# Performance work log

Measured on AMD Instinct MI355X. Metric: run time of the kernel, lower is better.

The kernel has to match this reference:

```python
import jax, jax.numpy as jnp
import numpy as np

B, S, H, D, DM = 2, 512, 8, 32, 256  # batch, seq_len, n_head, d_k, d_model


def setup_inputs() -> dict:
    key = jax.random.key(0)
    ks = jax.random.split(key, 8)
    scale = 0.02
    return {
        "hidden_states": jax.random.normal(ks[0], (B, S, DM), dtype=jnp.float32),
        "rpe": jax.random.normal(ks[1], (B, S, S, D), dtype=jnp.float32),
        "w_q": jax.random.normal(ks[2], (DM, H * D), dtype=jnp.float32) * scale,
        "w_k": jax.random.normal(ks[3], (DM, H * D), dtype=jnp.float32) * scale,
        "w_v": jax.random.normal(ks[4], (DM, H * D), dtype=jnp.float32) * scale,
        "fc_w": jax.random.normal(ks[5], (H * D, DM), dtype=jnp.float32) * scale,
        "fc_b": jnp.zeros((DM,), dtype=jnp.float32),
        "ln_w": jnp.ones((DM,), dtype=jnp.float32),
        "ln_b": jnp.zeros((DM,), dtype=jnp.float32),
        "station_num": 256,
    }


def reference(hidden_states, rpe, w_q, w_k, w_v, fc_w, fc_b, ln_w, ln_b, station_num):
    b, s, dm = hidden_states.shape
    d = rpe.shape[-1]
    h = w_q.shape[1] // d

    def heads(x, w):
        # (b, s, dm) @ (dm, h*d) -> (b, h, s, d)
        return (x @ w).reshape(b, s, h, d).transpose(0, 2, 1, 3)

    q = heads(hidden_states, w_q)
    k = heads(hidden_states, w_k)
    v = heads(hidden_states, w_v)

    # torch: (q.unsqueeze(2) * k.unsqueeze(3) * rpe.unsqueeze(1)).sum(-1)
    # scores[b,h,i,j] = sum_d q[b,h,j,d] * k[b,h,i,d] * rpe[b,i,j,d]
    scores = jnp.einsum('bhjd,bhid,bijd->bhij', q, k, rpe) / jnp.sqrt(jnp.float32(d))

    # shielded mask: column j visible if j < station_num, plus the diagonal
    col = jnp.arange(s) < station_num                  # (s,)
    mask = col[None, :] | jnp.eye(s, dtype=bool)        # (s, s)
    scores = jnp.where(mask[None, None], scores, jnp.float32(-1e10))

    attn = jax.nn.softmax(scores, axis=-1)              # (b, h, s, s)
    out = jnp.einsum('bhij,bhjd->bhid', attn, v)        # (b, h, s, d)
    out = out.transpose(0, 2, 1, 3).reshape(b, s, h * d)

    ctx = out @ fc_w + fc_b + hidden_states             # residual
    mu = jnp.mean(ctx, axis=-1, keepdims=True)
    var = jnp.mean(jnp.square(ctx - mu), axis=-1, keepdims=True)
    ctx = (ctx - mu) / jnp.sqrt(var + 1e-6) * ln_w + ln_b
    return ctx
```

## Files before the change

### kernel.cpp

```cpp
#include <hip/hip_runtime.h>
#include <hip/hip_bf16.h>

#define B_  2
#define S_  512
#define H_  8
#define D_  32
#define DM_ 256
#define HD_ 256
#define NROW 8
#define TI  2
#define CH  64

__global__ __launch_bounds__(256) void qkv_kernel(
    const float* __restrict__ hid, const float* __restrict__ wq,
    const float* __restrict__ wk, const float* __restrict__ wv,
    float* __restrict__ qo, float* __restrict__ ko, float* __restrict__ vo)
{
  __shared__ __align__(16) float hs[NROW][DM_];
  const int r0 = blockIdx.x * NROW;
  const float* w   = (blockIdx.y == 0) ? wq : (blockIdx.y == 1) ? wk : wv;
  float*       out = (blockIdx.y == 0) ? qo : (blockIdx.y == 1) ? ko : vo;
  const float mulf = (blockIdx.y == 0) ? 0.17677669529663687f : 1.0f;
  const int tid = threadIdx.x;

  for (int idx = tid; idx < NROW * DM_; idx += 256)
    hs[idx >> 8][idx & 255] = hid[r0 * DM_ + idx];
  __syncthreads();

  float acc[NROW] = {0.f, 0.f, 0.f, 0.f, 0.f, 0.f, 0.f, 0.f};
  const float* wp = w + tid;
  #pragma unroll 4
  for (int c4 = 0; c4 < DM_ / 4; ++c4) {
    const float w0 = wp[(4 * c4 + 0) * HD_];
    const float w1 = wp[(4 * c4 + 1) * HD_];
    const float w2 = wp[(4 * c4 + 2) * HD_];
    const float w3 = wp[(4 * c4 + 3) * HD_];
    #pragma unroll
    for (int r = 0; r < NROW; ++r) {
      const float4 hv = reinterpret_cast<const float4*>(&hs[r][0])[c4];
      acc[r] = fmaf(hv.x, w0, acc[r]);
      acc[r] = fmaf(hv.y, w1, acc[r]);
      acc[r] = fmaf(hv.z, w2, acc[r]);
      acc[r] = fmaf(hv.w, w3, acc[r]);
    }
  }
  const int h = tid >> 5, d = tid & 31;
  #pragma unroll
  for (int r = 0; r < NROW; ++r) {
    const int g = r0 + r;
    const int b = g >> 9, s = g & (S_ - 1);
    out[((b * H_ + h) * S_ + s) * D_ + d] = acc[r] * mulf;
  }
}

__device__ __forceinline__ float red4(float x) {
  int i;
  i = __builtin_amdgcn_mov_dpp(__float_as_int(x), 0xB1, 0xf, 0xf, true);
  x += __int_as_float(i);
  i = __builtin_amdgcn_mov_dpp(__float_as_int(x), 0x4E, 0xf, 0xf, true);
  x += __int_as_float(i);
  return x;
}

#define RSL(jj, c) (((jj) << 3) | ((c) ^ ((jj) & 7)))

__global__ __launch_bounds__(512, 4) void attn_fused_kernel(
    const float* __restrict__ rpe, const float* __restrict__ q_ws,
    const float* __restrict__ k_ws, const float* __restrict__ v_ws,
    const int* __restrict__ station_p, const float* __restrict__ fc_w,
    const float* __restrict__ fc_b, const float* __restrict__ hid,
    const float* __restrict__ ln_w, const float* __restrict__ ln_b,
    float* __restrict__ out)
{
  __shared__ __align__(16) float p_smem[TI][H_][S_];
  __shared__ __align__(16) float rpe_s[2][TI][CH * D_];
  __shared__ __align__(16) float ks[TI][H_ * D_];
  __shared__ __align__(16) float orow[TI][HD_];
  __shared__ float sums[TI][H_];
  __shared__ float redm[TI][4];
  __shared__ float redvr[TI][4];

  const int tid  = threadIdx.x;
  const int w    = tid >> 6, lane = tid & 63;
  const int j4   = lane >> 2, dq = lane & 3;
  const int j8   = lane >> 3, dc = lane & 7;
  const int n    = blockIdx.x;
  const int b    = n >> 8;
  const int i0   = (n & 255) * TI;
  const int HS   = S_ * D_;

  int station = station_p[0];
  station = station > S_ ? S_ : (station < 0 ? 0 : station);
  const bool dx0 = (i0 >= station);
  const bool dx1 = (i0 + 1 >= station);

  const float* qb = q_ws + (size_t)(b * H_) * S_ * D_;
  const float* kb = k_ws + (size_t)(b * H_) * S_ * D_;
  const float* vb = v_ws + (size_t)(b * H_) * S_ * D_;
  const float* rb0 = rpe + ((size_t)(b * S_ + i0) * S_) * D_;
  const float* rb1 = rpe + ((size_t)(b * S_ + i0 + 1) * S_) * D_;

  {
    const int ii = tid >> 8, rest = tid & 255;
    const int h = rest >> 5, d = rest & 31;
    ks[ii][rest] = kb[h * HS + (i0 + ii) * D_ + d];
  }
  const int nc = (station + CH - 1) >> 6;
  {
    const int jj = tid >> 3, cs = tid & 7;
    const int sl = RSL(jj, cs);
    if (nc > 0) {
      reinterpret_cast<float4*>(&rpe_s[0][0][0])[sl] =
          reinterpret_cast<const float4*>(rb0)[tid];
      reinterpret_cast<float4*>(&rpe_s[0][1][0])[sl] =
          reinterpret_cast<const float4*>(rb1)[tid];
    }
  }
  __syncthreads();

  const float4 k0a = *reinterpret_cast<const float4*>(&ks[0][w * D_ + dq * 8]);
  const float4 k0b = *reinterpret_cast<const float4*>(&ks[0][w * D_ + dq * 8 + 4]);
  const float4 k1a = *reinterpret_cast<const float4*>(&ks[1][w * D_ + dq * 8]);
  const float4 k1b = *reinterpret_cast<const float4*>(&ks[1][w * D_ + dq * 8 + 4]);
  const float* qh = qb + w * HS;
  float* ph0 = &p_smem[0][w][0];
  float* ph1 = &p_smem[1][w][0];

  for (int c = 0; c < nc; ++c) {
    if (c) __syncthreads();
    if (c + 1 < nc) {
      const int jj = tid >> 3, cs = tid & 7;
      const int sl = RSL(jj, cs);
      const int buf = (c + 1) & 1;
      reinterpret_cast<float4*>(&rpe_s[buf][0][0])[sl] =
          reinterpret_cast<const float4*>(rb0 + (c + 1) * CH * D_)[tid];
      reinterpret_cast<float4*>(&rpe_s[buf][1][0])[sl] =
          reinterpret_cast<const float4*>(rb1 + (c + 1) * CH * D_)[tid];
    }
    const float4* rs0 = reinterpret_cast<const float4*>(&rpe_s[c & 1][0][0]);
    const float4* rs1 = reinterpret_cast<const float4*>(&rpe_s[c & 1][1][0]);
    #pragma unroll
    for (int p = 0; p < CH / 16; ++p) {
      const int jl = p * 16 + j4;
      const int j  = c * CH + jl;
      const float4 q0 = *reinterpret_cast<const float4*>(qh + j * D_ + dq * 8);
      const float4 q1 = *reinterpret_cast<const float4*>(qh + j * D_ + dq * 8 + 4);
      const float4 ra0 = rs0[RSL(jl, 2 * dq)];
      const float4 ra1 = rs0[RSL(jl, 2 * dq + 1)];
      const float4 rb0v = rs1[RSL(jl, 2 * dq)];
      const float4 rb1v = rs1[RSL(jl, 2 * dq + 1)];
      float s0 = q0.x * k0a.x * ra0.x;
      s0 = fmaf(q0.y * k0a.y, ra0.y, s0);
      s0 = fmaf(q0.z * k0a.z, ra0.z, s0);
      s0 = fmaf(q0.w * k0a.w, ra0.w, s0);
      s0 = fmaf(q1.x * k0b.x, ra1.x, s0);
      s0 = fmaf(q1.y * k0b.y, ra1.y, s0);
      s0 = fmaf(q1.z * k0b.z, ra1.z, s0);
      s0 = fmaf(q1.w * k0b.w, ra1.w, s0);
      float s1 = q0.x * k1a.x * rb0v.x;
      s1 = fmaf(q0.y * k1a.y, rb0v.y, s1);
      s1 = fmaf(q0.z * k1a.z, rb0v.z, s1);
      s1 = fmaf(q0.w * k1a.w, rb0v.w, s1);
      s1 = fmaf(q1.x * k1b.x, rb1v.x, s1);
      s1 = fmaf(q1.y * k1b.y, rb1v.y, s1);
      s1 = fmaf(q1.z * k1b.z, rb1v.z, s1);
      s1 = fmaf(q1.w * k1b.w, rb1v.w, s1);
      s0 = red4(s0);
      s1 = red4(s1);
      if (dq == 0 && j < station) { ph0[j] = s0; ph1[j] = s1; }
    }
  }
  if (j4 == 0) {
    if (dx0) {
      const int i = i0;
      const float4 r0 = *reinterpret_cast<const float4*>(rb0 + i * D_ + dq * 8);
      const float4 r1 = *reinterpret_cast<const float4*>(rb0 + i * D_ + dq * 8 + 4);
      const float4 q0 = *reinterpret_cast<const float4*>(qh + i * D_ + dq * 8);
      const float4 q1 = *reinterpret_cast<const float4*>(qh + i * D_ + dq * 8 + 4);
      float s = q0.x * k0a.x * r0.x;
      s = fmaf(q0.y * k0a.y, r0.y, s);
      s = fmaf(q0.z * k0a.z, r0.z, s);
      s = fmaf(q0.w * k0a.w, r0.w, s);
      s = fmaf(q1.x * k0b.x, r1.x, s);
      s = fmaf(q1.y * k0b.y, r1.y, s);
      s = fmaf(q1.z * k0b.z, r1.z, s);
      s = fmaf(q1.w * k0b.w, r1.w, s);
      s = red4(s);
      if (dq == 0) ph0[i] = s;
    }
    if (dx1) {
      const int i = i0 + 1;
      const float4 r0 = *reinterpret_cast<const float4*>(rb1 + i * D_ + dq * 8);
      const float4 r1 = *reinterpret_cast<const float4*>(rb1 + i * D_ + dq * 8 + 4);
      const float4 q0 = *reinterpret_cast<const float4*>(qh + i * D_ + dq * 8);
      const float4 q1 = *reinterpret_cast<const float4*>(qh + i * D_ + dq * 8 + 4);
      float s = q0.x * k1a.x * r0.x;
      s = fmaf(q0.y * k1a.y, r0.y, s);
      s = fmaf(q0.z * k1a.z, r0.z, s);
      s = fmaf(q0.w * k1a.w, r0.w, s);
      s = fmaf(q1.x * k1b.x, r1.x, s);
      s = fmaf(q1.y * k1b.y, r1.y, s);
      s = fmaf(q1.z * k1b.z, r1.z, s);
      s = fmaf(q1.w * k1b.w, r1.w, s);
      s = red4(s);
      if (dq == 0) ph1[i] = s;
    }
  }
  __syncthreads();

  #pragma unroll
  for (int ii = 0; ii < TI; ++ii) {
    float* pr = &p_smem[ii][w][0];
    const int ig = i0 + ii;
    const bool dxi = (ig >= station);
    float m = -1e30f;
    for (int jj = lane; jj < station; jj += 64) m = fmaxf(m, pr[jj]);
    const float dv = dxi ? pr[ig] : -1e30f;
    m = fmaxf(m, dv);
    #pragma unroll
    for (int o = 32; o; o >>= 1) m = fmaxf(m, __shfl_xor(m, o, 64));
    float sum = 0.f;
    for (int jj = lane; jj < station; jj += 64) {
      const float e = __expf(pr[jj] - m);
      pr[jj] = e;
      sum += e;
    }
    #pragma unroll
    for (int o = 32; o; o >>= 1) sum += __shfl_xor(sum, o, 64);
    if (dxi) {
      const float e = __expf(dv - m);
      sum += e;
      if (lane == 0) pr[ig] = e;
    }
    if (lane == 0) sums[ii][w] = sum;
  }
  __syncthreads();

  float4 a0 = make_float4(0.f, 0.f, 0.f, 0.f);
  float4 a1 = make_float4(0.f, 0.f, 0.f, 0.f);
  {
    const float* vh = vb + w * HS;
    #pragma unroll 4
    for (int jb = 0; jb < station; jb += 8) {
      const int j  = jb + j8;
      const int jc = j < S_ ? j : S_ - 1;
      const float4 v4 = *reinterpret_cast<const float4*>(vh + jc * D_ + dc * 4);
      float pv0 = 0.f, pv1 = 0.f;
      if (j < station) { pv0 = ph0[j]; pv1 = ph1[j]; }
      a0.x = fmaf(pv0, v4.x, a0.x);
      a0.y = fmaf(pv0, v4.y, a0.y);
      a0.z = fmaf(pv0, v4.z, a0.z);
      a0.w = fmaf(pv0, v4.w, a0.w);
      a1.x = fmaf(pv1, v4.x, a1.x);
      a1.y = fmaf(pv1, v4.y, a1.y);
      a1.z = fmaf(pv1, v4.z, a1.z);
      a1.w = fmaf(pv1, v4.w, a1.w);
    }
  }
  #pragma unroll
  for (int o = 8; o <= 32; o <<= 1) {
    a0.x += __shfl_xor(a0.x, o, 64);
    a0.y += __shfl_xor(a0.y, o, 64);
    a0.z += __shfl_xor(a0.z, o, 64);
    a0.w += __shfl_xor(a0.w, o, 64);
    a1.x += __shfl_xor(a1.x, o, 64);
    a1.y += __shfl_xor(a1.y, o, 64);
    a1.z += __shfl_xor(a1.z, o, 64);
    a1.w += __shfl_xor(a1.w, o, 64);
  }
  if (j8 == 0) {
    if (dx0) {
      const float pv = ph0[i0];
      const float4 v4 = *reinterpret_cast<const float4*>(vb + w * HS + i0 * D_ + dc * 4);
      a0.x = fmaf(pv, v4.x, a0.x);
      a0.y = fmaf(pv, v4.y, a0.y);
      a0.z = fmaf(pv, v4.z, a0.z);
      a0.w = fmaf(pv, v4.w, a0.w);
    }
    if (dx1) {
      const float pv = ph1[i0 + 1];
      const float4 v4 = *reinterpret_cast<const float4*>(vb + w * HS + (i0 + 1) * D_ + dc * 4);
      a1.x = fmaf(pv, v4.x, a1.x);
      a1.y = fmaf(pv, v4.y, a1.y);
      a1.z = fmaf(pv, v4.z, a1.z);
      a1.w = fmaf(pv, v4.w, a1.w);
    }
    const float inv0 = 1.f / sums[0][w];
    const float inv1 = 1.f / sums[1][w];
    a0.x *= inv0; a0.y *= inv0; a0.z *= inv0; a0.w *= inv0;
    a1.x *= inv1; a1.y *= inv1; a1.z *= inv1; a1.w *= inv1;
    reinterpret_cast<float4*>(&orow[0][w * D_])[dc] = a0;
    reinterpret_cast<float4*>(&orow[1][w * D_])[dc] = a1;
  }
  __syncthreads();

  float f0 = 0.f, f1 = 0.f;
  if (tid < DM_) {
    const float* wp = fc_w + tid;
    #pragma unroll 8
    for (int n4 = 0; n4 < HD_ / 4; ++n4) {
      const float4 o0 = reinterpret_cast<const float4*>(&orow[0][0])[n4];
      const float4 o1 = reinterpret_cast<const float4*>(&orow[1][0])[n4];
      const float w0 = wp[(4 * n4 + 0) * DM_];
      const float w1 = wp[(4 * n4 + 1) * DM_];
      const float w2 = wp[(4 * n4 + 2) * DM_];
      const float w3 = wp[(4 * n4 + 3) * DM_];
      f0 = fmaf(o0.x, w0, f0); f1 = fmaf(o1.x, w0, f1);
      f0 = fmaf(o0.y, w1, f0); f1 = fmaf(o1.y, w1, f1);
      f0 = fmaf(o0.z, w2, f0); f1 = fmaf(o1.z, w2, f1);
      f0 = fmaf(o0.w, w3, f0); f1 = fmaf(o1.w, w3, f1);
    }
    const float bias = fc_b[tid];
    f0 += bias + hid[(size_t)(b * S_ + i0) * DM_ + tid];
    f1 += bias + hid[(size_t)(b * S_ + i0 + 1) * DM_ + tid];
    float s0 = f0, s1 = f1;
    #pragma unroll
    for (int o = 32; o; o >>= 1) {
      s0 += __shfl_xor(s0, o, 64);
      s1 += __shfl_xor(s1, o, 64);
    }
    if (lane == 0) { redm[0][w] = s0; redm[1][w] = s1; }
  }
  __syncthreads();
  const float mu0 = (redm[0][0] + redm[0][1] + redm[0][2] + redm[0][3]) * (1.f / DM_);
  const float mu1 = (redm[1][0] + redm[1][1] + redm[1][2] + redm[1][3]) * (1.f / DM_);
  const float d0 = f0 - mu0, d1 = f1 - mu1;
  if (tid < DM_) {
    float s0 = d0 * d0, s1 = d1 * d1;
    #pragma unroll
    for (int o = 32; o; o >>= 1) {
      s0 += __shfl_xor(s0, o, 64);
      s1 += __shfl_xor(s1, o, 64);
    }
    if (lane == 0) { redvr[0][w] = s0; redvr[1][w] = s1; }
  }
  __syncthreads();
  if (tid < DM_) {
    const float v0 = (redvr[0][0] + redvr[0][1] + redvr[0][2] + redvr[0][3]) * (1.f / DM_);
    const float v1 = (redvr[1][0] + redvr[1][1] + redvr[1][2] + redvr[1][3]) * (1.f / DM_);
    const float lw = ln_w[tid], lb = ln_b[tid];
    out[(size_t)(b * S_ + i0) * DM_ + tid]     = d0 * rsqrtf(v0 + 1e-6f) * lw + lb;
    out[(size_t)(b * S_ + i0 + 1) * DM_ + tid] = d1 * rsqrtf(v1 + 1e-6f) * lw + lb;
  }
}

extern "C" void kernel_launch(void* const* d_in, const int* in_sizes, int n_in,
                              void* d_out, int out_size, void* d_ws, size_t ws_size,
                              hipStream_t stream) {
  const float* hid = (const float*)d_in[0];
  const float* rpe = (const float*)d_in[1];
  const float* wq  = (const float*)d_in[2];
  const float* wk  = (const float*)d_in[3];
  const float* wv  = (const float*)d_in[4];
  const float* fcw = (const float*)d_in[5];
  const float* fcb = (const float*)d_in[6];
  const float* lnw = (const float*)d_in[7];
  const float* lnb = (const float*)d_in[8];
  const int* station = (const int*)d_in[9];
  float* out = (float*)d_out;

  const size_t per = (size_t)B_ * H_ * S_ * D_;
  float* q_ws = (float*)d_ws;
  float* k_ws = q_ws + per;
  float* v_ws = k_ws + per;

  dim3 gA(B_ * S_ / NROW, 3);
  qkv_kernel<<<gA, 256, 0, stream>>>(hid, wq, wk, wv, q_ws, k_ws, v_ws);
  attn_fused_kernel<<<B_ * S_ / TI, 512, 0, stream>>>(
      rpe, q_ws, k_ws, v_ws, station, fcw, fcb, hid, lnw, lnb, out);
}
```

Measured before the change: 149.1 us.

## Halve RPE chunk, double QKV rows per block, raise occupancy, swizzle block order

The rpe staging chunk is halved so each thread loads one float4 per chunk instead of two, which cuts shared memory per block. The attention kernel's launch bound is raised to target 6 blocks per SM. Block indices are remapped so consecutive blocks interleave across rows and batches. The QKV projection kernel now handles 16 rows per block with less unrolling, so each weight load is reused across more rows. The risks are register spills from the tighter launch bound and more barrier passes per chunk because chunks are smaller.

```diff
diff --git a/kernel.cpp b/kernel.cpp
--- a/kernel.cpp
+++ b/kernel.cpp
@@ -7,9 +7,9 @@
 #define D_  32
 #define DM_ 256
 #define HD_ 256
-#define NROW 8
+#define NROW 16
 #define TI  2
-#define CH  64
+#define CH  32
 
 __global__ __launch_bounds__(256) void qkv_kernel(
     const float* __restrict__ hid, const float* __restrict__ wq,
@@ -27,9 +27,11 @@
     hs[idx >> 8][idx & 255] = hid[r0 * DM_ + idx];
   __syncthreads();
 
-  float acc[NROW] = {0.f, 0.f, 0.f, 0.f, 0.f, 0.f, 0.f, 0.f};
+  float acc[NROW];
+  #pragma unroll
+  for (int r = 0; r < NROW; ++r) acc[r] = 0.f;
   const float* wp = w + tid;
-  #pragma unroll 4
+  #pragma unroll 2
   for (int c4 = 0; c4 < DM_ / 4; ++c4) {
     const float w0 = wp[(4 * c4 + 0) * HD_];
     const float w1 = wp[(4 * c4 + 1) * HD_];
@@ -64,7 +66,7 @@
 
 #define RSL(jj, c) (((jj) << 3) | ((c) ^ ((jj) & 7)))
 
-__global__ __launch_bounds__(512, 4) void attn_fused_kernel(
+__global__ __launch_bounds__(512, 6) void attn_fused_kernel(
     const float* __restrict__ rpe, const float* __restrict__ q_ws,
     const float* __restrict__ k_ws, const float* __restrict__ v_ws,
     const int* __restrict__ station_p, const float* __restrict__ fc_w,
@@ -84,7 +86,7 @@
   const int w    = tid >> 6, lane = tid & 63;
   const int j4   = lane >> 2, dq = lane & 3;
   const int j8   = lane >> 3, dc = lane & 7;
-  const int n    = blockIdx.x;
+  const int n    = ((blockIdx.x & 7) << 6) | (blockIdx.x >> 3);
   const int b    = n >> 8;
   const int i0   = (n & 255) * TI;
   const int HS   = S_ * D_;
@@ -105,16 +107,14 @@
     const int h = rest >> 5, d = rest & 31;
     ks[ii][rest] = kb[h * HS + (i0 + ii) * D_ + d];
   }
-  const int nc = (station + CH - 1) >> 6;
-  {
-    const int jj = tid >> 3, cs = tid & 7;
-    const int sl = RSL(jj, cs);
-    if (nc > 0) {
-      reinterpret_cast<float4*>(&rpe_s[0][0][0])[sl] =
-          reinterpret_cast<const float4*>(rb0)[tid];
-      reinterpret_cast<float4*>(&rpe_s[0][1][0])[sl] =
-          reinterpret_cast<const float4*>(rb1)[tid];
-    }
+  const int nc = (station + CH - 1) / CH;
+  const int sii = tid >> 8, sidx = tid & 255;
+  const int sjj = sidx >> 3, scs = sidx & 7;
+  const int ssl = RSL(sjj, scs);
+  const float* srb = sii ? rb1 : rb0;
+  if (nc > 0) {
+    reinterpret_cast<float4*>(&rpe_s[0][sii][0])[ssl] =
+        reinterpret_cast<const float4*>(srb)[sidx];
   }
   __syncthreads();
 
@@ -129,13 +129,9 @@
   for (int c = 0; c < nc; ++c) {
     if (c) __syncthreads();
     if (c + 1 < nc) {
-      const int jj = tid >> 3, cs = tid & 7;
-      const int sl = RSL(jj, cs);
       const int buf = (c + 1) & 1;
-      reinterpret_cast<float4*>(&rpe_s[buf][0][0])[sl] =
-          reinterpret_cast<const float4*>(rb0 + (c + 1) * CH * D_)[tid];
-      reinterpret_cast<float4*>(&rpe_s[buf][1][0])[sl] =
-          reinterpret_cast<const float4*>(rb1 + (c + 1) * CH * D_)[tid];
+      reinterpret_cast<float4*>(&rpe_s[buf][sii][0])[ssl] =
+          reinterpret_cast<const float4*>(srb + (c + 1) * CH * D_)[sidx];
     }
     const float4* rs0 = reinterpret_cast<const float4*>(&rpe_s[c & 1][0][0]);
     const float4* rs1 = reinterpret_cast<const float4*>(&rpe_s[c & 1][1][0]);
@@ -147,8 +143,8 @@
       const float4 q1 = *reinterpret_cast<const float4*>(qh + j * D_ + dq * 8 + 4);
       const float4 ra0 = rs0[RSL(jl, 2 * dq)];
       const float4 ra1 = rs0[RSL(jl, 2 * dq + 1)];
-      const float4 rb0v = rs1[RSL(jl, 2 * dq)];
-      const float4 rb1v = rs1[RSL(jl, 2 * dq + 1)];
+      const float4 rc0 = rs1[RSL(jl, 2 * dq)];
+      const float4 rc1 = rs1[RSL(jl, 2 * dq + 1)];
       float s0 = q0.x * k0a.x * ra0.x;
       s0 = fmaf(q0.y * k0a.y, ra0.y, s0);
       s0 = fmaf(q0.z * k0a.z, ra0.z, s0);
@@ -157,14 +153,14 @@
       s0 = fmaf(q1.y * k0b.y, ra1.y, s0);
       s0 = fmaf(q1.z * k0b.z, ra1.z, s0);
       s0 = fmaf(q1.w * k0b.w, ra1.w, s0);
-      float s1 = q0.x * k1a.x * rb0v.x;
-      s1 = fmaf(q0.y * k1a.y, rb0v.y, s1);
-      s1 = fmaf(q0.z * k1a.z, rb0v.z, s1);
-      s1 = fmaf(q0.w * k1a.w, rb0v.w, s1);
-      s1 = fmaf(q1.x * k1b.x, rb1v.x, s1);
-      s1 = fmaf(q1.y * k1b.y, rb1v.y, s1);
-      s1 = fmaf(q1.z * k1b.z, rb1v.z, s1);
-      s1 = fmaf(q1.w * k1b.w, rb1v.w, s1);
+      float s1 = q0.x * k1a.x * rc0.x;
+      s1 = fmaf(q0.y * k1a.y, rc0.y, s1);
+      s1 = fmaf(q0.z * k1a.z, rc0.z, s1);
+      s1 = fmaf(q0.w * k1a.w, rc0.w, s1);
+      s1 = fmaf(q1.x * k1b.x, rc1.x, s1);
+      s1 = fmaf(q1.y * k1b.y, rc1.y, s1);
+      s1 = fmaf(q1.z * k1b.z, rc1.z, s1);
+      s1 = fmaf(q1.w * k1b.w, rc1.w, s1);
       s0 = red4(s0);
       s1 = red4(s1);
       if (dq == 0 && j < station) { ph0[j] = s0; ph1[j] = s1; }
```

After: 177.6 us. +19.1%, slower.
